# Optimization experiments

Hardware: AMD Instinct MI355X
Metric: run time of the kernel (lower is better)

The kernel has to match this reference:

```python
import jax, jax.numpy as jnp
import numpy as np

N_NODES = 100000
N_EDGES = 1600000
N_REL = 8
IN_CH = 16
HID_CH = 32
OUT_CH = 2


def setup_inputs() -> dict:
    key = jax.random.key(0)
    ks = jax.random.split(key, 9)
    x = jax.random.normal(ks[0], (N_NODES, IN_CH), dtype=jnp.float32)
    edge_index = jax.random.randint(ks[1], (2, N_EDGES), 0, N_NODES, dtype=jnp.int64)
    edge_type = jax.random.randint(ks[2], (N_EDGES,), 0, N_REL, dtype=jnp.int64)
    s = 0.1
    W1 = jax.random.normal(ks[3], (N_REL, IN_CH, HID_CH), dtype=jnp.float32) * s
    root1 = jax.random.normal(ks[4], (IN_CH, HID_CH), dtype=jnp.float32) * s
    b1 = jnp.zeros((HID_CH,), dtype=jnp.float32)
    W2 = jax.random.normal(ks[5], (N_REL, HID_CH, OUT_CH), dtype=jnp.float32) * s
    root2 = jax.random.normal(ks[6], (HID_CH, OUT_CH), dtype=jnp.float32) * s
    b2 = jnp.zeros((OUT_CH,), dtype=jnp.float32)
    return {"x": x, "edge_index": edge_index, "edge_type": edge_type,
            "W1": W1, "root1": root1, "b1": b1,
            "W2": W2, "root2": root2, "b2": b2}


def rgcn_conv(x, W, Wroot, b, src, dst, rel, num_nodes, num_rel):
    """PyG RGCNConv: per-relation mean aggregation + root weight + bias."""
    # Transform all nodes by all relation weights up front: [N, R, H]
    xW = jnp.einsum('nf,rfh->nrh', x, W)
    msg = xW[src, rel]                       # [E, H] gather per edge
    # mean per (dst, relation): normalize each message by its group size
    key = dst * num_rel + rel                # combined segment key
    ones = jnp.ones(rel.shape, dtype=x.dtype)
    cnt = jax.ops.segment_sum(ones, key, num_segments=num_nodes * num_rel)
    norm = 1.0 / jnp.maximum(cnt, 1.0)
    msg = msg * norm[key][:, None]
    agg = jax.ops.segment_sum(msg, dst, num_segments=num_nodes)  # sum over relations
    return agg + x @ Wroot + b


def reference(x, edge_index, edge_type, W1, root1, b1, W2, root2, b2):
    src, dst = edge_index[0], edge_index[1]
    h = rgcn_conv(x, W1, root1, b1, src, dst, edge_type, N_NODES, N_REL)
    h = jax.nn.relu(h)
    # dropout is identity in eval mode (training=False)
    out = rgcn_conv(h, W2, root2, b2, src, dst, edge_type, N_NODES, N_REL)
    return jax.nn.log_softmax(out, axis=1)
```

## Files before the change

### kernel.cpp

```cpp
#include <hip/hip_runtime.h>
#include <math.h>

#define N_REL  8
#define IN_CH  16
#define HID_CH 32
#define OUT_CH 2

#define BIN_BITS  9
#define BIN_NODES 512
#define KPB       (BIN_NODES * N_REL)
#define NCHUNK    192
#define XW_TILE   64

static __device__ __forceinline__ unsigned short f2b(float f) {
    unsigned int u = __float_as_uint(f);
    u = (u + 0x7FFFu + ((u >> 16) & 1u)) >> 16;
    return (unsigned short)u;
}
static __device__ __forceinline__ float b2f(unsigned short s) {
    return __uint_as_float(((unsigned int)s) << 16);
}

__global__ __launch_bounds__(256) void prep_kernel(const float* __restrict__ x,
                                                   const float* __restrict__ W1,
                                                   unsigned short* __restrict__ xW16,
                                                   const int* __restrict__ dst,
                                                   int* __restrict__ H,
                                                   int N, int E, int nbins,
                                                   int chunksz, int nxw) {
    __shared__ float sx[XW_TILE * IN_CH];
    __shared__ int hist[256];
    int t = threadIdx.x;

    if ((int)blockIdx.x < nxw) {
        int node0 = blockIdx.x * XW_TILE;
        {
            int i4 = node0 * 4 + t;
            float4 v = make_float4(0.f, 0.f, 0.f, 0.f);
            if (i4 < N * 4) v = ((const float4*)x)[i4];
            ((float4*)sx)[t] = v;
        }
        __syncthreads();

        int r = t >> 5, c = t & 31;
        float w[IN_CH];
#pragma unroll
        for (int f = 0; f < IN_CH; ++f)
            w[f] = W1[(r * IN_CH + f) * HID_CH + c];

        int lim = N - node0; if (lim > XW_TILE) lim = XW_TILE;
        for (int ni = 0; ni < lim; ++ni) {
            const float4* xs = (const float4*)(sx + ni * IN_CH);
            float4 v0 = xs[0], v1 = xs[1], v2 = xs[2], v3 = xs[3];
            float a;
            a  = v0.x * w[0]  + v0.y * w[1]  + v0.z * w[2]  + v0.w * w[3];
            a += v1.x * w[4]  + v1.y * w[5]  + v1.z * w[6]  + v1.w * w[7];
            a += v2.x * w[8]  + v2.y * w[9]  + v2.z * w[10] + v2.w * w[11];
            a += v3.x * w[12] + v3.y * w[13] + v3.z * w[14] + v3.w * w[15];
            xW16[(node0 + ni) * (N_REL * HID_CH) + t] = f2b(a);
        }
    } else {
        int chunk = blockIdx.x - nxw;
        int e0 = chunk * chunksz;
        int e1 = e0 + chunksz; if (e1 > E) e1 = E;

        for (int i = t; i < nbins; i += 256) hist[i] = 0;
        __syncthreads();
        for (int e = e0 + t; e < e1; e += 256)
            atomicAdd(&hist[dst[e] >> BIN_BITS], 1);
        __syncthreads();
        for (int i = t; i < nbins; i += 256)
            H[i * NCHUNK + chunk] = hist[i];
    }
}

__global__ __launch_bounds__(1024) void scan_a_kernel(int* __restrict__ ptr,
                                                      int* __restrict__ blksum, int M) {
    int i = blockIdx.x * 1024 + threadIdx.x;
    int val = (i < M) ? ptr[i] : 0;
    int lane = threadIdx.x & 63;
    int wid  = threadIdx.x >> 6;

    int v = val;
#pragma unroll
    for (int off = 1; off < 64; off <<= 1) {
        int u = __shfl_up(v, off, 64);
        if (lane >= off) v += u;
    }

    __shared__ int wsum[16];
    if (lane == 63) wsum[wid] = v;
    __syncthreads();

    if (wid == 0) {
        int worig = (lane < 16) ? wsum[lane] : 0;
        int wv = worig;
#pragma unroll
        for (int off = 1; off < 16; off <<= 1) {
            int u = __shfl_up(wv, off, 64);
            if (lane >= off) wv += u;
        }
        if (lane < 16) wsum[lane] = wv - worig;
        if (lane == 15) blksum[blockIdx.x] = wv;
    }
    __syncthreads();

    if (i < M) ptr[i] = (v - val) + wsum[wid];
}

__global__ void scan_b_kernel(int* __restrict__ blksum, int nb) {
    int lane = threadIdx.x & 63;
    int run = 0;
    for (int base = 0; base < nb; base += 64) {
        int i = base + lane;
        int val = (i < nb) ? blksum[i] : 0;
        int v = val;
#pragma unroll
        for (int off = 1; off < 64; off <<= 1) {
            int u = __shfl_up(v, off, 64);
            if (lane >= off) v += u;
        }
        if (i < nb) blksum[i] = run + (v - val);
        run += __shfl(v, 63, 64);
    }
}

__global__ __launch_bounds__(256) void part_scatter_kernel(const int* __restrict__ src,
                                                           const int* __restrict__ dst,
                                                           const int* __restrict__ rel,
                                                           const int* __restrict__ Hs,
                                                           const int* __restrict__ blksum,
                                                           int* __restrict__ be,
                                                           int E, int nbins, int chunksz) {
    __shared__ int base[256];
    __shared__ int fil[256];
    int chunk = blockIdx.x;
    int e0 = chunk * chunksz;
    int e1 = e0 + chunksz; if (e1 > E) e1 = E;

    for (int i = threadIdx.x; i < nbins; i += 256) {
        int idx = i * NCHUNK + chunk;
        base[i] = Hs[idx] + blksum[idx >> 10];
        fil[i]  = 0;
    }
    __syncthreads();

    for (int e = e0 + threadIdx.x; e < e1; e += 256) {
        int d = dst[e];
        int b = d >> BIN_BITS;
        int slot = base[b] + atomicAdd(&fil[b], 1);
        be[slot] = ((d & (BIN_NODES - 1)) << 20) | (rel[e] << 17) | src[e];
    }
}

__global__ __launch_bounds__(256) void bin_build_kernel(const int* __restrict__ be,
                                                        const int* __restrict__ Hs,
                                                        const int* __restrict__ blksum,
                                                        int* __restrict__ ends,
                                                        int* __restrict__ csr,
                                                        float* __restrict__ einv,
                                                        int E, int nbins) {
    int b  = blockIdx.x;
    int i0 = b * NCHUNK;
    int s0 = Hs[i0] + blksum[i0 >> 10];
    int s1 = E;
    if (b + 1 < nbins) {
        int i1 = (b + 1) * NCHUNK;
        s1 = Hs[i1] + blksum[i1 >> 10];
    }
    int t  = threadIdx.x;

    __shared__ int cnt[KPB];
    __shared__ int off[KPB];
    __shared__ int fil[KPB];
    __shared__ int ws[4];

    for (int i = t; i < KPB; i += 256) { cnt[i] = 0; fil[i] = 0; }
    __syncthreads();

    for (int p = s0 + t; p < s1; p += 256)
        atomicAdd(&cnt[be[p] >> 17], 1);
    __syncthreads();

    int kbase = t * 16;
    int loc[16];
    int sum = 0;
#pragma unroll
    for (int i = 0; i < 16; ++i) { loc[i] = sum; sum += cnt[kbase + i]; }

    int lane = t & 63, wid = t >> 6;
    int v = sum;
#pragma unroll
    for (int o = 1; o < 64; o <<= 1) {
        int u = __shfl_up(v, o, 64);
        if (lane >= o) v += u;
    }
    if (lane == 63) ws[wid] = v;
    __syncthreads();
    int woff = 0;
    for (int i = 0; i < wid; ++i) woff += ws[i];
    int excl = woff + (v - sum);
#pragma unroll
    for (int i = 0; i < 16; ++i) off[kbase + i] = excl + loc[i];
    __syncthreads();

    for (int i = t; i < KPB; i += 256)
        ends[b * KPB + i] = s0 + off[i] + cnt[i];

    for (int p = s0 + t; p < s1; p += 256) {
        int pk = be[p];
        int k  = pk >> 17;
        int slot = s0 + off[k] + atomicAdd(&fil[k], 1);
        csr[slot]  = ((pk & 0x1FFFF) << 3) | (k & 7);
        einv[slot] = 1.0f / (float)cnt[k];
    }
}

#define STAGE_SW2(sw2, W2, root2)                                              \
    for (int i = threadIdx.x; i < 288; i += 256) {                             \
        int f = i / 9, j = i - f * 9;                                          \
        float a, bb;                                                           \
        if (j < 8) { a = W2[(j * HID_CH + f) * 2]; bb = W2[(j * HID_CH + f) * 2 + 1]; } \
        else       { a = root2[f * 2];             bb = root2[f * 2 + 1]; }    \
        sw2[i] = make_float2(a, bb);                                           \
    }

#define EPILOGUE_V2(sw2, hval, node, c, hW16, hroot, b2)                       \
    {                                                                          \
        int g  = (c >> 4) << 4;                                                \
        int jj = c & 15; if (jj > 8) jj = 8;                                   \
        float o0 = 0.0f, o1 = 0.0f;                                            \
        _Pragma("unroll")                                                      \
        for (int k = 0; k < 16; ++k) {                                         \
            float hf = __shfl(hval, g + k, 32);                                \
            float2 wv = sw2[(g + k) * 9 + jj];                                 \
            o0 = fmaf(hf, wv.x, o0);                                           \
            o1 = fmaf(hf, wv.y, o1);                                           \
        }                                                                      \
        o0 += __shfl_xor(o0, 16, 32);                                          \
        o1 += __shfl_xor(o1, 16, 32);                                          \
        if (c < 8) {                                                           \
            hW16[((node) << 3) + c] = ((unsigned)f2b(o1) << 16) | f2b(o0);     \
        } else if (c == 8) {                                                   \
            *(float2*)(hroot + ((long)(node) << 1)) =                          \
                make_float2(o0 + b2[0], o1 + b2[1]);                           \
        }                                                                      \
    }

__global__ __launch_bounds__(256) void l1_fused_kernel(const float* __restrict__ x,
                                                       const int* __restrict__ csr,
                                                       const float* __restrict__ einv,
                                                       const int* __restrict__ ends,
                                                       const unsigned short* __restrict__ xW16,
                                                       const float* __restrict__ root1,
                                                       const float* __restrict__ b1,
                                                       const float* __restrict__ W2,
                                                       const float* __restrict__ root2,
                                                       const float* __restrict__ b2,
                                                       unsigned int* __restrict__ hW16,
                                                       float* __restrict__ hroot, int N) {
    __shared__ float2 sw2[32 * 9];
    STAGE_SW2(sw2, W2, root2)
    __syncthreads();

    int gid  = blockIdx.x * 256 + threadIdx.x;
    int node = gid >> 5;
    int c    = gid & 31;
    if (node >= N) return;

    int p0 = (node > 0) ? __ldg(&ends[node * N_REL - 1]) : 0;
    int p1 = __ldg(&ends[node * N_REL + N_REL - 1]);

    float acc0 = 0.0f, acc1 = 0.0f;
    int p = p0;
    for (; p + 7 < p1; p += 8) {
        int v0 = csr[p],     v1 = csr[p + 1], v2 = csr[p + 2], v3 = csr[p + 3];
        int v4 = csr[p + 4], v5 = csr[p + 5], v6 = csr[p + 6], v7 = csr[p + 7];
        float i0 = einv[p],     i1 = einv[p + 1], i2 = einv[p + 2], i3 = einv[p + 3];
        float i4 = einv[p + 4], i5 = einv[p + 5], i6 = einv[p + 6], i7 = einv[p + 7];
        float a0 = b2f(xW16[(v0 << 5) + c]);
        float a1 = b2f(xW16[(v1 << 5) + c]);
        float a2 = b2f(xW16[(v2 << 5) + c]);
        float a3 = b2f(xW16[(v3 << 5) + c]);
        float a4 = b2f(xW16[(v4 << 5) + c]);
        float a5 = b2f(xW16[(v5 << 5) + c]);
        float a6 = b2f(xW16[(v6 << 5) + c]);
        float a7 = b2f(xW16[(v7 << 5) + c]);
        acc0 = fmaf(a0, i0, acc0);
        acc1 = fmaf(a1, i1, acc1);
        acc0 = fmaf(a2, i2, acc0);
        acc1 = fmaf(a3, i3, acc1);
        acc0 = fmaf(a4, i4, acc0);
        acc1 = fmaf(a5, i5, acc1);
        acc0 = fmaf(a6, i6, acc0);
        acc1 = fmaf(a7, i7, acc1);
    }
    for (; p + 3 < p1; p += 4) {
        int v0 = csr[p], v1 = csr[p + 1], v2 = csr[p + 2], v3 = csr[p + 3];
        float i0 = einv[p], i1 = einv[p + 1], i2 = einv[p + 2], i3 = einv[p + 3];
        acc0 = fmaf(b2f(xW16[(v0 << 5) + c]), i0, acc0);
        acc1 = fmaf(b2f(xW16[(v1 << 5) + c]), i1, acc1);
        acc0 = fmaf(b2f(xW16[(v2 << 5) + c]), i2, acc0);
        acc1 = fmaf(b2f(xW16[(v3 << 5) + c]), i3, acc1);
    }
    if (p + 1 < p1) {
        int v0 = csr[p], v1 = csr[p + 1];
        acc0 = fmaf(b2f(xW16[(v0 << 5) + c]), einv[p], acc0);
        acc1 = fmaf(b2f(xW16[(v1 << 5) + c]), einv[p + 1], acc1);
        p += 2;
    }
    if (p < p1)
        acc0 = fmaf(b2f(xW16[(csr[p] << 5) + c]), einv[p], acc0);

    const float4* xs = (const float4*)(x + ((long)node << 4));
    float4 v0 = xs[0], v1 = xs[1], v2 = xs[2], v3 = xs[3];
    const float* wr = root1 + c;
    float acc = acc0 + acc1 + b1[c];
    acc += v0.x * wr[0]   + v0.y * wr[32]  + v0.z * wr[64]  + v0.w * wr[96];
    acc += v1.x * wr[128] + v1.y * wr[160] + v1.z * wr[192] + v1.w * wr[224];
    acc += v2.x * wr[256] + v2.y * wr[288] + v2.z * wr[320] + v2.w * wr[352];
    acc += v3.x * wr[384] + v3.y * wr[416] + v3.z * wr[448] + v3.w * wr[480];
    float hval = fmaxf(acc, 0.0f);

    EPILOGUE_V2(sw2, hval, node, c, hW16, hroot, b2)
}

__global__ __launch_bounds__(256) void l1_fb_kernel(const float* __restrict__ x,
                                                    const int* __restrict__ csr,
                                                    const float* __restrict__ einv,
                                                    const int* __restrict__ ends,
                                                    const float* __restrict__ W1,
                                                    const float* __restrict__ root1,
                                                    const float* __restrict__ b1,
                                                    const float* __restrict__ W2,
                                                    const float* __restrict__ root2,
                                                    const float* __restrict__ b2,
                                                    unsigned int* __restrict__ hW16,
                                                    float* __restrict__ hroot, int N) {
    __shared__ float sW[N_REL * IN_CH * HID_CH];
    __shared__ float2 sw2[32 * 9];
    for (int i = threadIdx.x; i < N_REL * IN_CH * HID_CH; i += 256) sW[i] = W1[i];
    STAGE_SW2(sw2, W2, root2)
    __syncthreads();

    int gid  = blockIdx.x * 256 + threadIdx.x;
    int node = gid >> 5;
    int c    = gid & 31;
    if (node >= N) return;

    int p0 = (node > 0) ? __ldg(&ends[node * N_REL - 1]) : 0;
    int p1 = __ldg(&ends[node * N_REL + N_REL - 1]);

    float acc = 0.0f;
    for (int p = p0; p < p1; ++p) {
        int v = csr[p];
        int s = v >> 3, r = v & 7;
        const float4* xs = (const float4*)(x + ((long)s << 4));
        float4 q0 = xs[0], q1 = xs[1], q2 = xs[2], q3 = xs[3];
        const float* w = sW + ((r * IN_CH) * HID_CH) + c;
        float a;
        a  = q0.x * w[0]   + q0.y * w[32]  + q0.z * w[64]  + q0.w * w[96];
        a += q1.x * w[128] + q1.y * w[160] + q1.z * w[192] + q1.w * w[224];
        a += q2.x * w[256] + q2.y * w[288] + q2.z * w[320] + q2.w * w[352];
        a += q3.x * w[384] + q3.y * w[416] + q3.z * w[448] + q3.w * w[480];
        acc = fmaf(a, einv[p], acc);
    }

    const float4* xs = (const float4*)(x + ((long)node << 4));
    float4 v0 = xs[0], v1 = xs[1], v2 = xs[2], v3 = xs[3];
    const float* wr = root1 + c;
    acc += b1[c];
    acc += v0.x * wr[0]   + v0.y * wr[32]  + v0.z * wr[64]  + v0.w * wr[96];
    acc += v1.x * wr[128] + v1.y * wr[160] + v1.z * wr[192] + v1.w * wr[224];
    acc += v2.x * wr[256] + v2.y * wr[288] + v2.z * wr[320] + v2.w * wr[352];
    acc += v3.x * wr[384] + v3.y * wr[416] + v3.z * wr[448] + v3.w * wr[480];
    float hval = fmaxf(acc, 0.0f);

    EPILOGUE_V2(sw2, hval, node, c, hW16, hroot, b2)
}

__global__ __launch_bounds__(256) void l2_flat_kernel(const int* __restrict__ csr,
                                                      const float* __restrict__ einv,
                                                      const int* __restrict__ ends,
                                                      const unsigned int* __restrict__ hW16,
                                                      const float* __restrict__ hroot,
                                                      float* __restrict__ out, int N) {
    int gid  = blockIdx.x * 256 + threadIdx.x;
    int node = gid >> 4;
    int l    = gid & 15;
    if (node >= N) return;

    int p0 = (node > 0) ? __ldg(&ends[node * N_REL - 1]) : 0;
    int p1 = __ldg(&ends[node * N_REL + N_REL - 1]);

    float o0 = 0.0f, o1 = 0.0f;
    for (int p = p0 + l; p < p1; p += 16) {
        int v = csr[p];
        float w = einv[p];
        unsigned u = hW16[v];
        o0 = fmaf(b2f((unsigned short)u), w, o0);
        o1 = fmaf(b2f((unsigned short)(u >> 16)), w, o1);
    }

#pragma unroll
    for (int m = 1; m < 16; m <<= 1) {
        o0 += __shfl_xor(o0, m, 64);
        o1 += __shfl_xor(o1, m, 64);
    }

    if (l == 0) {
        float2 rt = *(const float2*)(hroot + ((long)node << 1));
        o0 += rt.x; o1 += rt.y;
        float mx = fmaxf(o0, o1);
        float lg = mx + logf(__expf(o0 - mx) + __expf(o1 - mx));
        *(float2*)(out + ((long)node << 1)) = make_float2(o0 - lg, o1 - lg);
    }
}

extern "C" void kernel_launch(void* const* d_in, const int* in_sizes, int n_in,
                              void* d_out, int out_size, void* d_ws, size_t ws_size,
                              hipStream_t stream) {
    const float* x     = (const float*)d_in[0];
    const int*   eidx  = (const int*)d_in[1];
    const int*   etype = (const int*)d_in[2];
    const float* W1    = (const float*)d_in[3];
    const float* root1 = (const float*)d_in[4];
    const float* b1    = (const float*)d_in[5];
    const float* W2    = (const float*)d_in[6];
    const float* root2 = (const float*)d_in[7];
    const float* b2    = (const float*)d_in[8];
    float* out = (float*)d_out;

    const int N = in_sizes[0] / IN_CH;
    const int E = in_sizes[2];
    const int nbins   = (N + BIN_NODES - 1) >> BIN_BITS;
    const int chunksz = (E + NCHUNK - 1) / NCHUNK;
    const int M2      = nbins * NCHUNK;
    const int* src = eidx;
    const int* dst = eidx + E;

    char* wp = (char*)d_ws;
    auto take = [&](size_t bytes) {
        char* p = wp;
        wp += (bytes + 63) & ~(size_t)63;
        return p;
    };
    int*   H      = (int*)take((size_t)M2 * sizeof(int));
    int*   blksum = (int*)take(4096 * sizeof(int));
    int*   ends   = (int*)take((size_t)nbins * KPB * sizeof(int));
    int*   csr    = (int*)take((size_t)E * sizeof(int));
    float* einv   = (float*)take((size_t)E * sizeof(float));
    int*   be     = (int*)take((size_t)E * sizeof(int));
    unsigned int* hW16 = (unsigned int*)take((size_t)N * N_REL * sizeof(unsigned int));
    float* hroot  = (float*)take((size_t)N * 2 * sizeof(float));
    unsigned short* xW16 = (unsigned short*)take((size_t)N * N_REL * HID_CH * sizeof(unsigned short));
    bool use_xw = ((size_t)(wp - (char*)d_ws) <= ws_size);

    const int B = 256;
    const int nb = (M2 + 1023) / 1024;
    const int nxw = use_xw ? (N + XW_TILE - 1) / XW_TILE : 0;

    prep_kernel<<<nxw + NCHUNK, B, 0, stream>>>(x, W1, xW16, dst, H, N, E, nbins, chunksz, nxw);
    scan_a_kernel<<<nb, 1024, 0, stream>>>(H, blksum, M2);
    scan_b_kernel<<<1, 64, 0, stream>>>(blksum, nb);
    part_scatter_kernel<<<NCHUNK, B, 0, stream>>>(src, dst, etype, H, blksum, be, E, nbins, chunksz);
    bin_build_kernel<<<nbins, B, 0, stream>>>(be, H, blksum, ends, csr, einv, E, nbins);

    if (use_xw) {
        l1_fused_kernel<<<(N * 32 + B - 1) / B, B, 0, stream>>>(
            x, csr, einv, ends, xW16, root1, b1, W2, root2, b2, hW16, hroot, N);
    } else {
        l1_fb_kernel<<<(N * 32 + B - 1) / B, B, 0, stream>>>(
            x, csr, einv, ends, W1, root1, b1, W2, root2, b2, hW16, hroot, N);
    }

    l2_flat_kernel<<<(N * 16 + B - 1) / B, B, 0, stream>>>(csr, einv, ends, hW16, hroot, out, N);
}
```

Measured before the change: 157.0 us.

## Use 64 lanes per node in layer 1 and compact per-node row pointers

Layer 1 now gives each node a full 64-lane wavefront, with two 32-lane halves splitting the edge list by parity and combining their sums with a cross-half shuffle. This doubles memory-level parallelism for the gathers. The layer-2 weights move from shared memory into per-lane registers, which drops the LDS staging and its block barrier. The per-(node,relation) ends array is replaced by a compact per-node rowptr, shrinking that write and the pointer reads. The cost is twice as many threads, redundant root/x computation in both halves, and more registers.

```diff
diff --git a/kernel.cpp b/kernel.cpp
--- a/kernel.cpp
+++ b/kernel.cpp
@@ -156,7 +156,7 @@
 __global__ __launch_bounds__(256) void bin_build_kernel(const int* __restrict__ be,
                                                         const int* __restrict__ Hs,
                                                         const int* __restrict__ blksum,
-                                                        int* __restrict__ ends,
+                                                        int* __restrict__ rowptr,
                                                         int* __restrict__ csr,
                                                         float* __restrict__ einv,
                                                         int E, int nbins) {
@@ -205,7 +205,9 @@
     __syncthreads();
 
     for (int i = t; i < KPB; i += 256)
-        ends[b * KPB + i] = s0 + off[i] + cnt[i];
+        if ((i & 7) == 7)
+            rowptr[b * BIN_NODES + (i >> 3) + 1] = s0 + off[i] + cnt[i];
+    if (b == 0 && t == 0) rowptr[0] = 0;
 
     for (int p = s0 + t; p < s1; p += 256) {
         int pk = be[p];
@@ -216,41 +218,10 @@
     }
 }
 
-#define STAGE_SW2(sw2, W2, root2)                                              \
-    for (int i = threadIdx.x; i < 288; i += 256) {                             \
-        int f = i / 9, j = i - f * 9;                                          \
-        float a, bb;                                                           \
-        if (j < 8) { a = W2[(j * HID_CH + f) * 2]; bb = W2[(j * HID_CH + f) * 2 + 1]; } \
-        else       { a = root2[f * 2];             bb = root2[f * 2 + 1]; }    \
-        sw2[i] = make_float2(a, bb);                                           \
-    }
-
-#define EPILOGUE_V2(sw2, hval, node, c, hW16, hroot, b2)                       \
-    {                                                                          \
-        int g  = (c >> 4) << 4;                                                \
-        int jj = c & 15; if (jj > 8) jj = 8;                                   \
-        float o0 = 0.0f, o1 = 0.0f;                                            \
-        _Pragma("unroll")                                                      \
-        for (int k = 0; k < 16; ++k) {                                         \
-            float hf = __shfl(hval, g + k, 32);                                \
-            float2 wv = sw2[(g + k) * 9 + jj];                                 \
-            o0 = fmaf(hf, wv.x, o0);                                           \
-            o1 = fmaf(hf, wv.y, o1);                                           \
-        }                                                                      \
-        o0 += __shfl_xor(o0, 16, 32);                                          \
-        o1 += __shfl_xor(o1, 16, 32);                                          \
-        if (c < 8) {                                                           \
-            hW16[((node) << 3) + c] = ((unsigned)f2b(o1) << 16) | f2b(o0);     \
-        } else if (c == 8) {                                                   \
-            *(float2*)(hroot + ((long)(node) << 1)) =                          \
-                make_float2(o0 + b2[0], o1 + b2[1]);                           \
-        }                                                                      \
-    }
-
 __global__ __launch_bounds__(256) void l1_fused_kernel(const float* __restrict__ x,
                                                        const int* __restrict__ csr,
                                                        const float* __restrict__ einv,
-                                                       const int* __restrict__ ends,
+                                                       const int* __restrict__ rowptr,
                                                        const unsigned short* __restrict__ xW16,
                                                        const float* __restrict__ root1,
                                                        const float* __restrict__ b1,
@@ -259,25 +230,33 @@
                                                        const float* __restrict__ b2,
                                                        unsigned int* __restrict__ hW16,
                                                        float* __restrict__ hroot, int N) {
-    __shared__ float2 sw2[32 * 9];
-    STAGE_SW2(sw2, W2, root2)
-    __syncthreads();
-
     int gid  = blockIdx.x * 256 + threadIdx.x;
-    int node = gid >> 5;
-    int c    = gid & 31;
+    int node = gid >> 6;
+    int l    = gid & 63;
+    int c    = l & 31;
+    int par  = l >> 5;
     if (node >= N) return;
 
-    int p0 = (node > 0) ? __ldg(&ends[node * N_REL - 1]) : 0;
-    int p1 = __ldg(&ends[node * N_REL + N_REL - 1]);
+    int g  = l >> 4;
+    int jj = l & 15; if (jj > 8) jj = 8;
+    float2 w2r[8];
+#pragma unroll
+    for (int k = 0; k < 8; ++k) {
+        int ch = g * 8 + k;
+        w2r[k] = (jj < 8) ? *(const float2*)(W2 + (jj * HID_CH + ch) * 2)
+                          : *(const float2*)(root2 + ch * 2);
+    }
+
+    int p0 = rowptr[node];
+    int p1 = rowptr[node + 1];
 
     float acc0 = 0.0f, acc1 = 0.0f;
-    int p = p0;
-    for (; p + 7 < p1; p += 8) {
-        int v0 = csr[p],     v1 = csr[p + 1], v2 = csr[p + 2], v3 = csr[p + 3];
-        int v4 = csr[p + 4], v5 = csr[p + 5], v6 = csr[p + 6], v7 = csr[p + 7];
-        float i0 = einv[p],     i1 = einv[p + 1], i2 = einv[p + 2], i3 = einv[p + 3];
-        float i4 = einv[p + 4], i5 = einv[p + 5], i6 = einv[p + 6], i7 = einv[p + 7];
+    int p = p0 + par;
+    for (; p + 14 < p1; p += 16) {
+        int v0 = csr[p],      v1 = csr[p + 2],  v2 = csr[p + 4],  v3 = csr[p + 6];
+        int v4 = csr[p + 8],  v5 = csr[p + 10], v6 = csr[p + 12], v7 = csr[p + 14];
+        float i0 = einv[p],      i1 = einv[p + 2],  i2 = einv[p + 4],  i3 = einv[p + 6];
+        float i4 = einv[p + 8],  i5 = einv[p + 10], i6 = einv[p + 12], i7 = einv[p + 14];
         float a0 = b2f(xW16[(v0 << 5) + c]);
         float a1 = b2f(xW16[(v1 << 5) + c]);
         float a2 = b2f(xW16[(v2 << 5) + c]);
@@ -295,40 +274,53 @@
         acc0 = fmaf(a6, i6, acc0);
         acc1 = fmaf(a7, i7, acc1);
     }
-    for (; p + 3 < p1; p += 4) {
-        int v0 = csr[p], v1 = csr[p + 1], v2 = csr[p + 2], v3 = csr[p + 3];
-        float i0 = einv[p], i1 = einv[p + 1], i2 = einv[p + 2], i3 = einv[p + 3];
+    for (; p + 6 < p1; p += 8) {
+        int v0 = csr[p], v1 = csr[p + 2], v2 = csr[p + 4], v3 = csr[p + 6];
+        float i0 = einv[p], i1 = einv[p + 2], i2 = einv[p + 4], i3 = einv[p + 6];
         acc0 = fmaf(b2f(xW16[(v0 << 5) + c]), i0, acc0);
         acc1 = fmaf(b2f(xW16[(v1 << 5) + c]), i1, acc1);
         acc0 = fmaf(b2f(xW16[(v2 << 5) + c]), i2, acc0);
         acc1 = fmaf(b2f(xW16[(v3 << 5) + c]), i3, acc1);
     }
-    if (p + 1 < p1) {
-        int v0 = csr[p], v1 = csr[p + 1];
-        acc0 = fmaf(b2f(xW16[(v0 << 5) + c]), einv[p], acc0);
-        acc1 = fmaf(b2f(xW16[(v1 << 5) + c]), einv[p + 1], acc1);
-        p += 2;
-    }
-    if (p < p1)
+    for (; p < p1; p += 2)
         acc0 = fmaf(b2f(xW16[(csr[p] << 5) + c]), einv[p], acc0);
+
+    float acc = acc0 + acc1;
+    acc += __shfl_xor(acc, 32, 64);
 
     const float4* xs = (const float4*)(x + ((long)node << 4));
     float4 v0 = xs[0], v1 = xs[1], v2 = xs[2], v3 = xs[3];
     const float* wr = root1 + c;
-    float acc = acc0 + acc1 + b1[c];
+    acc += b1[c];
     acc += v0.x * wr[0]   + v0.y * wr[32]  + v0.z * wr[64]  + v0.w * wr[96];
     acc += v1.x * wr[128] + v1.y * wr[160] + v1.z * wr[192] + v1.w * wr[224];
     acc += v2.x * wr[256] + v2.y * wr[288] + v2.z * wr[320] + v2.w * wr[352];
     acc += v3.x * wr[384] + v3.y * wr[416] + v3.z * wr[448] + v3.w * wr[480];
     float hval = fmaxf(acc, 0.0f);
 
-    EPILOGUE_V2(sw2, hval, node, c, hW16, hroot, b2)
+    float o0 = 0.0f, o1 = 0.0f;
+#pragma unroll
+    for (int k = 0; k < 8; ++k) {
+        float hf = __shfl(hval, g * 8 + k, 64);
+        o0 = fmaf(hf, w2r[k].x, o0);
+        o1 = fmaf(hf, w2r[k].y, o1);
+    }
+    o0 += __shfl_xor(o0, 16, 64);
+    o1 += __shfl_xor(o1, 16, 64);
+    o0 += __shfl_xor(o0, 32, 64);
+    o1 += __shfl_xor(o1, 32, 64);
+
+    if (l < 8) {
+        hW16[(node << 3) + l] = ((unsigned)f2b(o1) << 16) | f2b(o0);
+    } else if (l == 8) {
+        *(float2*)(hroot + ((long)node << 1)) = make_float2(o0 + b2[0], o1 + b2[1]);
+    }
 }
 
 __global__ __launch_bounds__(256) void l1_fb_kernel(const float* __restrict__ x,
                                                     const int* __restrict__ csr,
                                                     const float* __restrict__ einv,
-                                                    const int* __restrict__ ends,
+                                                    const int* __restrict__ rowptr,
                                                     const float* __restrict__ W1,
                                                     const float* __restrict__ root1,
                                                     const float* __restrict__ b1,
@@ -338,25 +330,35 @@
                                                     unsigned int* __restrict__ hW16,
                                                     float* __restrict__ hroot, int N) {
     __shared__ float sW[N_REL * IN_CH * HID_CH];
-    __shared__ float2 sw2[32 * 9];
     for (int i = threadIdx.x; i < N_REL * IN_CH * HID_CH; i += 256) sW[i] = W1[i];
-    STAGE_SW2(sw2, W2, root2)
     __syncthreads();
 
     int gid  = blockIdx.x * 256 + threadIdx.x;
-    int node = gid >> 5;
-    int c    = gid & 31;
+    int node = gid >> 6;
+    int l    = gid & 63;
+    int c    = l & 31;
+    int par  = l >> 5;
     if (node >= N) return;
 
-    int p0 = (node > 0) ? __ldg(&ends[node * N_REL - 1]) : 0;
-    int p1 = __ldg(&ends[node * N_REL + N_REL - 1]);
+    int g  = l >> 4;
+    int jj = l & 15; if (jj > 8) jj = 8;
+    float2 w2r[8];
+#pragma unroll
+    for (int k = 0; k < 8; ++k) {
+        int ch = g * 8 + k;
+        w2r[k] = (jj < 8) ? *(const float2*)(W2 + (jj * HID_CH + ch) * 2)
+                          : *(const float2*)(root2 + ch * 2);
+    }
+
+    int p0 = rowptr[node];
+    int p1 = rowptr[node + 1];
 
     float acc = 0.0f;
-    for (int p = p0; p < p1; ++p) {
+    for (int p = p0 + par; p < p1; p += 2) {
         int v = csr[p];
         int s = v >> 3, r = v & 7;
-        const float4* xs = (const float4*)(x + ((long)s << 4));
-        float4 q0 = xs[0], q1 = xs[1], q2 = xs[2], q3 = xs[3];
+        const float4* xsv = (const float4*)(x + ((long)s << 4));
+        float4 q0 = xsv[0], q1 = xsv[1], q2 = xsv[2], q3 = xsv[3];
         const float* w = sW + ((r * IN_CH) * HID_CH) + c;
         float a;
         a  = q0.x * w[0]   + q0.y * w[32]  + q0.z * w[64]  + q0.w * w[96];
@@ -365,6 +367,7 @@
         a += q3.x * w[384] + q3.y * w[416] + q3.z * w[448] + q3.w * w[480];
         acc = fmaf(a, einv[p], acc);
     }
+    acc += __shfl_xor(acc, 32, 64);
 
     const float4* xs = (const float4*)(x + ((long)node << 4));
     float4 v0 = xs[0], v1 = xs[1], v2 = xs[2], v3 = xs[3];
@@ -376,12 +379,28 @@
     acc += v3.x * wr[384] + v3.y * wr[416] + v3.z * wr[448] + v3.w * wr[480];
     float hval = fmaxf(acc, 0.0f);
 
-    EPILOGUE_V2(sw2, hval, node, c, hW16, hroot, b2)
+    float o0 = 0.0f, o1 = 0.0f;
+#pragma unroll
+    for (int k = 0; k < 8; ++k) {
+        float hf = __shfl(hval, g * 8 + k, 64);
+        o0 = fmaf(hf, w2r[k].x, o0);
+        o1 = fmaf(hf, w2r[k].y, o1);
+    }
+    o0 += __shfl_xor(o0, 16, 64);
+    o1 += __shfl_xor(o1, 16, 64);
+    o0 += __shfl_xor(o0, 32, 64);
+    o1 += __shfl_xor(o1, 32, 64);
+
+    if (l < 8) {
+        hW16[(node << 3) + l] = ((unsigned)f2b(o1) << 16) | f2b(o0);
+    } else if (l == 8) {
+        *(float2*)(hroot + ((long)node << 1)) = make_float2(o0 + b2[0], o1 + b2[1]);
+    }
 }
 
 __global__ __launch_bounds__(256) void l2_flat_kernel(const int* __restrict__ csr,
                                                       const float* __restrict__ einv,
-                                                      const int* __restrict__ ends,
+                                                      const int* __restrict__ rowptr,
                                                       const unsigned int* __restrict__ hW16,
                                                       const float* __restrict__ hroot,
                                                       float* __restrict__ out, int N) {
@@ -390,8 +409,8 @@
     int l    = gid & 15;
     if (node >= N) return;
 
-    int p0 = (node > 0) ? __ldg(&ends[node * N_REL - 1]) : 0;
-    int p1 = __ldg(&ends[node * N_REL + N_REL - 1]);
+    int p0 = rowptr[node];
+    int p1 = rowptr[node + 1];
 
     float o0 = 0.0f, o1 = 0.0f;
     for (int p = p0 + l; p < p1; p += 16) {
@@ -447,7 +466,7 @@
     };
     int*   H      = (int*)take((size_t)M2 * sizeof(int));
     int*   blksum = (int*)take(4096 * sizeof(int));
-    int*   ends   = (int*)take((size_t)nbins * KPB * sizeof(int));
+    int*   rowptr = (int*)take((size_t)(nbins * BIN_NODES + 1) * sizeof(int));
     int*   csr    = (int*)take((size_t)E * sizeof(int));
     float* einv   = (float*)take((size_t)E * sizeof(float));
     int*   be     = (int*)take((size_t)E * sizeof(int));
@@ -464,15 +483,15 @@
     scan_a_kernel<<<nb, 1024, 0, stream>>>(H, blksum, M2);
     scan_b_kernel<<<1, 64, 0, stream>>>(blksum, nb);
     part_scatter_kernel<<<NCHUNK, B, 0, stream>>>(src, dst, etype, H, blksum, be, E, nbins, chunksz);
-    bin_build_kernel<<<nbins, B, 0, stream>>>(be, H, blksum, ends, csr, einv, E, nbins);
+    bin_build_kernel<<<nbins, B, 0, stream>>>(be, H, blksum, rowptr, csr, einv, E, nbins);
 
     if (use_xw) {
-        l1_fused_kernel<<<(N * 32 + B - 1) / B, B, 0, stream>>>(
-            x, csr, einv, ends, xW16, root1, b1, W2, root2, b2, hW16, hroot, N);
+        l1_fused_kernel<<<(N * 64 + B - 1) / B, B, 0, stream>>>(
+            x, csr, einv, rowptr, xW16, root1, b1, W2, root2, b2, hW16, hroot, N);
     } else {
-        l1_fb_kernel<<<(N * 32 + B - 1) / B, B, 0, stream>>>(
-            x, csr, einv, ends, W1, root1, b1, W2, root2, b2, hW16, hroot, N);
-    }
-
-    l2_flat_kernel<<<(N * 16 + B - 1) / B, B, 0, stream>>>(csr, einv, ends, hW16, hroot, out, N);
-}
+        l1_fb_kernel<<<(N * 64 + B - 1) / B, B, 0, stream>>>(
+            x, csr, einv, rowptr, W1, root1, b1, W2, root2, b2, hW16, hroot, N);
+    }
+
+    l2_flat_kernel<<<(N * 16 + B - 1) / B, B, 0, stream>>>(csr, einv, rowptr, hW16, hroot, out, N);
+}
```

Result: slower. 207.2 us (+32.0%).
